# Kernel tuning notes

Measured on AMD Instinct MI355X. Metric: run time of the kernel, lower is better.

## Reference

```python
import jax, jax.numpy as jnp
import numpy as np

D_K = 64

def setup_inputs() -> dict:
    key = jax.random.key(0)
    k1, k2, k3 = jax.random.split(key, 3)
    B, H, S, d = 4, 16, 2048, D_K
    Q = jax.random.normal(k1, (B, H, S, d), dtype=jnp.float32)
    K = jax.random.normal(k2, (B, H, S, d), dtype=jnp.float32)
    V = jax.random.normal(k3, (B, H, S, d), dtype=jnp.float32)
    attn_mask = jnp.ones((1, 1, S, S), dtype=jnp.float32)
    return {"Q": Q, "K": K, "V": V, "attn_mask": attn_mask}

def reference(Q, K, V, attn_mask):
    # scores = Q K^T / sqrt(d_k)  -> [B, H, S, S]
    scale = 1.0 / np.sqrt(D_K).astype(np.float32)
    scores = jnp.einsum('bhqd,bhkd->bhqk', Q, K) * scale
    # unnormalized exp (NO max-subtraction, faithful to original)
    scores = jnp.exp(scores)
    # multiplicative mask applied POST-exp
    scores = scores * attn_mask
    # manual sum-normalization with eps
    attn = scores / (jnp.sum(scores, axis=-1, keepdims=True) + 1e-08)
    context = jnp.einsum('bhqk,bhkd->bhqd', attn, V)
    return (context, attn)
```

## Files before the change

kernel.cpp:

```cpp
#include <hip/hip_runtime.h>

#define S_LEN 2048
#define D_KD  64
#define NKT   32
#define NBH   64
#define KSEG  4

typedef __attribute__((ext_vector_type(8))) short short8;
typedef __attribute__((ext_vector_type(4))) float f32x4;

__device__ __forceinline__ unsigned short f2bf(float f) {
    unsigned u = __builtin_bit_cast(unsigned, f);
    return (unsigned short)((u + 0x7fffu + ((u >> 16) & 1u)) >> 16);
}

__device__ __forceinline__ void ldsbar() {
    asm volatile("s_waitcnt lgkmcnt(0)" ::: "memory");
    __builtin_amdgcn_s_barrier();
}
__device__ __forceinline__ void ldswait() {
    asm volatile("s_waitcnt lgkmcnt(0)" ::: "memory");
    __builtin_amdgcn_sched_barrier(0);
}

__device__ __forceinline__ unsigned swz(int row, int bytecol) {
    return (unsigned)(row * 128 + bytecol) ^
           (((((unsigned)row & 7u) ^ ((unsigned)row >> 3)) & 7u) << 4);
}

__device__ __forceinline__ void load_rm(const float* __restrict__ g,
                                        float4 r[4], int tid) {
#pragma unroll
    for (int j = 0; j < 4; j++) r[j] = *(const float4*)(g + j * 1024 + tid * 4);
}
__device__ __forceinline__ void write_rm(const float4 r[4],
                                         unsigned char* lds, int tid) {
#pragma unroll
    for (int j = 0; j < 4; j++) {
        int idx = j * 1024 + tid * 4;
        int row = idx >> 6, col = idx & 63;
        ushort4 b = make_ushort4(f2bf(r[j].x), f2bf(r[j].y), f2bf(r[j].z), f2bf(r[j].w));
        *(ushort4*)(lds + swz(row, col * 2)) = b;
    }
}
__device__ __forceinline__ void load_tr(const float* __restrict__ g,
                                        float4 r[4], int tid) {
    const int br = tid >> 4, bc = tid & 15;
    const float* gp = g + (4 * br) * 64 + 4 * bc;
#pragma unroll
    for (int j = 0; j < 4; j++) r[j] = *(const float4*)(gp + j * 64);
}
__device__ __forceinline__ void write_tr(const float4 r[4],
                                         unsigned char* lds, int tid) {
    const int br = tid >> 4, bc = tid & 15;
    ushort4 c;
    c = make_ushort4(f2bf(r[0].x), f2bf(r[1].x), f2bf(r[2].x), f2bf(r[3].x));
    *(ushort4*)(lds + swz(4 * bc + 0, 8 * br)) = c;
    c = make_ushort4(f2bf(r[0].y), f2bf(r[1].y), f2bf(r[2].y), f2bf(r[3].y));
    *(ushort4*)(lds + swz(4 * bc + 1, 8 * br)) = c;
    c = make_ushort4(f2bf(r[0].z), f2bf(r[1].z), f2bf(r[2].z), f2bf(r[3].z));
    *(ushort4*)(lds + swz(4 * bc + 2, 8 * br)) = c;
    c = make_ushort4(f2bf(r[0].w), f2bf(r[1].w), f2bf(r[2].w), f2bf(r[3].w));
    *(ushort4*)(lds + swz(4 * bc + 3, 8 * br)) = c;
}
__device__ __forceinline__ void stage_rm(const float* __restrict__ g,
                                         unsigned char* lds, int tid) {
    float4 r[4];
    load_rm(g, r, tid);
    write_rm(r, lds, tid);
}

__device__ __forceinline__ void qkt(const unsigned char* Qs, const unsigned char* Ks,
                                    int wv, int lr, int lg, f32x4 acc[4]) {
    short8 a0 = *(const short8*)(Qs + swz(16 * wv + lr, 16 * lg));
    short8 a1 = *(const short8*)(Qs + swz(16 * wv + lr, 16 * lg + 64));
#pragma unroll
    for (int nt = 0; nt < 4; nt++) {
        short8 b0 = *(const short8*)(Ks + swz(16 * nt + lr, 16 * lg));
        short8 b1 = *(const short8*)(Ks + swz(16 * nt + lr, 16 * lg + 64));
        acc[nt] = __builtin_amdgcn_mfma_f32_16x16x32_bf16(a0, b0, acc[nt], 0, 0, 0);
        acc[nt] = __builtin_amdgcn_mfma_f32_16x16x32_bf16(a1, b1, acc[nt], 0, 0, 0);
    }
}

__global__ __launch_bounds__(256) void attn_ctx(
    const float* __restrict__ Q, const float* __restrict__ K,
    const float* __restrict__ V, const float* __restrict__ M,
    float* __restrict__ out, float* __restrict__ invg) {
    __shared__ unsigned char Qs[8192];
    __shared__ unsigned char Ks[8192];
    __shared__ unsigned char Vs[8192];
    __shared__ unsigned char Ps[8192];

    const int tid = threadIdx.x;
    const int wv = tid >> 6, lane = tid & 63, lr = lane & 15, lg = lane >> 4;
    const int blk = blockIdx.x;
    const int bh = (blk & 7) * 8 + (blk >> 8);
    const int qt = (blk >> 3) & 31;

    const float* Qg = Q + ((size_t)bh * S_LEN + qt * 64) * D_KD;
    const float* Kg = K + (size_t)bh * S_LEN * D_KD;
    const float* Vg = V + (size_t)bh * S_LEN * D_KD;
    float* ctxg = out + ((size_t)bh * S_LEN + qt * 64) * D_KD;
    const float* Mg = M + (size_t)(qt * 64) * S_LEN;

    stage_rm(Qg, Qs, tid);

    f32x4 accc[4] = {};
    float rs[4] = {0.f, 0.f, 0.f, 0.f};

    float4 kreg[4], vreg[4];
    load_rm(Kg, kreg, tid);
    load_tr(Vg, vreg, tid);

    for (int t = 0; t < NKT; t++) {
        write_rm(kreg, Ks, tid);
        write_tr(vreg, Vs, tid);
        ldsbar();

        if (t + 1 < NKT) {
            load_rm(Kg + (size_t)(t + 1) * 64 * D_KD, kreg, tid);
            load_tr(Vg + (size_t)(t + 1) * 64 * D_KD, vreg, tid);
        }

        float mreg[4][4];
#pragma unroll
        for (int r = 0; r < 4; r++) {
            const float* mrow = Mg + (size_t)(16 * wv + 4 * lg + r) * S_LEN + t * 64;
#pragma unroll
            for (int nt = 0; nt < 4; nt++) mreg[r][nt] = mrow[16 * nt + lr];
        }

        f32x4 acc[4] = {};
        qkt(Qs, Ks, wv, lr, lg, acc);

#pragma unroll
        for (int r = 0; r < 4; r++) {
            const int row = 16 * wv + 4 * lg + r;
#pragma unroll
            for (int nt = 0; nt < 4; nt++) {
                float e = __expf(acc[nt][r] * 0.125f) * mreg[r][nt];
                rs[r] += e;
                *(unsigned short*)(Ps + swz(row, (16 * nt + lr) * 2)) = f2bf(e);
            }
        }
        ldswait();

#pragma unroll
        for (int kt = 0; kt < 2; kt++) {
            short8 pa = *(const short8*)(Ps + swz(16 * wv + lr, 16 * lg + 64 * kt));
#pragma unroll
            for (int nt = 0; nt < 4; nt++) {
                short8 vb = *(const short8*)(Vs + swz(16 * nt + lr, 16 * lg + 64 * kt));
                accc[nt] = __builtin_amdgcn_mfma_f32_16x16x32_bf16(pa, vb, accc[nt], 0, 0, 0);
            }
        }
        ldsbar();
    }

    float inv[4];
#pragma unroll
    for (int r = 0; r < 4; r++) {
        float v = rs[r];
        v += __shfl_xor(v, 1);
        v += __shfl_xor(v, 2);
        v += __shfl_xor(v, 4);
        v += __shfl_xor(v, 8);
        inv[r] = 1.0f / (v + 1e-8f);
    }

#pragma unroll
    for (int r = 0; r < 4; r++) {
        const int row = 16 * wv + 4 * lg + r;
#pragma unroll
        for (int nt = 0; nt < 4; nt++)
            ctxg[(size_t)row * D_KD + 16 * nt + lr] = accc[nt][r] * inv[r];
    }

    if (lr == 0) {
#pragma unroll
        for (int r = 0; r < 4; r++)
            invg[(size_t)bh * S_LEN + qt * 64 + 16 * wv + 4 * lg + r] = inv[r];
    }
}

__global__ __launch_bounds__(256) void attn_mat(
    const float* __restrict__ Q, const float* __restrict__ K,
    const float* __restrict__ M, const float* __restrict__ invg,
    float* __restrict__ out) {
    __shared__ unsigned char Qs[8192];
    __shared__ unsigned char Ks[8192];

    const int tid = threadIdx.x;
    const int wv = tid >> 6, lane = tid & 63, lr = lane & 15, lg = lane >> 4;
    const int ks = blockIdx.x & (KSEG - 1);
    const int qt = (blockIdx.x >> 2) & 31;
    const int bh = blockIdx.x >> 7;

    const float* Qg = Q + ((size_t)bh * S_LEN + qt * 64) * D_KD;
    const float* Kg = K + (size_t)bh * S_LEN * D_KD;
    const float* Mg = M + (size_t)(qt * 64) * S_LEN;
    float* attng = out + (size_t)NBH * S_LEN * D_KD +
                   (size_t)bh * S_LEN * S_LEN + (size_t)(qt * 64) * S_LEN;

    stage_rm(Qg, Qs, tid);

    float inv[4];
#pragma unroll
    for (int r = 0; r < 4; r++)
        inv[r] = invg[(size_t)bh * S_LEN + qt * 64 + 16 * wv + 4 * lg + r];

    const int nt_kt = S_LEN / (64 * KSEG);
    const float* Kseg = Kg + (size_t)(ks * (S_LEN / KSEG)) * D_KD;

    float4 kreg[4];
    load_rm(Kseg, kreg, tid);

    for (int kt = 0; kt < nt_kt; kt++) {
        const int key0 = ks * (S_LEN / KSEG) + kt * 64;
        write_rm(kreg, Ks, tid);
        ldsbar();

        if (kt + 1 < nt_kt)
            load_rm(Kseg + (size_t)(kt + 1) * 64 * D_KD, kreg, tid);

        float mreg[4][4];
#pragma unroll
        for (int r = 0; r < 4; r++) {
            const float* mrow = Mg + (size_t)(16 * wv + 4 * lg + r) * S_LEN + key0;
#pragma unroll
            for (int nt = 0; nt < 4; nt++) mreg[r][nt] = mrow[16 * nt + lr];
        }

        f32x4 acc[4] = {};
        qkt(Qs, Ks, wv, lr, lg, acc);

#pragma unroll
        for (int r = 0; r < 4; r++) {
            const int row = 16 * wv + 4 * lg + r;
            float* arow = attng + (size_t)row * S_LEN + key0;
#pragma unroll
            for (int nt = 0; nt < 4; nt++) {
                float e = __expf(acc[nt][r] * 0.125f) * mreg[r][nt] * inv[r];
                __builtin_nontemporal_store(e, arow + 16 * nt + lr);
            }
        }
        ldsbar();
    }
}

extern "C" void kernel_launch(void* const* d_in, const int* in_sizes, int n_in,
                              void* d_out, int out_size, void* d_ws, size_t ws_size,
                              hipStream_t stream) {
    const float* Q = (const float*)d_in[0];
    const float* K = (const float*)d_in[1];
    const float* V = (const float*)d_in[2];
    const float* M = (const float*)d_in[3];
    float* out = (float*)d_out;
    float* invg = (float*)d_ws;
    attn_ctx<<<dim3(NBH * 32), dim3(256), 0, stream>>>(Q, K, V, M, out, invg);
    attn_mat<<<dim3(NBH * 32 * KSEG), dim3(256), 0, stream>>>(Q, K, M, invg, out);
}
```

Baseline: 453.7 us.

## Pre-convert K/V to swizzled bf16 images in workspace before attention kernels

Adds a conversion kernel that converts K to bf16 and V to transposed bf16, writing both in the swizzled LDS tile layout into workspace. The attention kernels then copy those tiles straight into LDS with 16-byte loads instead of reloading fp32 and converting on every Q tile. The context kernel also keeps Q fragments in registers rather than staging them through LDS. This removes the repeated fp32 K/V reads and conversions, at the cost of one extra launch and a workspace round trip, and it falls back to the old path when workspace is too small.

```diff
diff --git a/kernel.cpp b/kernel.cpp
--- a/kernel.cpp
+++ b/kernel.cpp
@@ -13,6 +13,14 @@
     unsigned u = __builtin_bit_cast(unsigned, f);
     return (unsigned short)((u + 0x7fffu + ((u >> 16) & 1u)) >> 16);
 }
+__device__ __forceinline__ short8 pack8(float4 a, float4 b) {
+    short8 r;
+    r[0] = (short)f2bf(a.x); r[1] = (short)f2bf(a.y);
+    r[2] = (short)f2bf(a.z); r[3] = (short)f2bf(a.w);
+    r[4] = (short)f2bf(b.x); r[5] = (short)f2bf(b.y);
+    r[6] = (short)f2bf(b.z); r[7] = (short)f2bf(b.w);
+    return r;
+}
 
 __device__ __forceinline__ void ldsbar() {
     asm volatile("s_waitcnt lgkmcnt(0)" ::: "memory");
@@ -34,13 +42,13 @@
     for (int j = 0; j < 4; j++) r[j] = *(const float4*)(g + j * 1024 + tid * 4);
 }
 __device__ __forceinline__ void write_rm(const float4 r[4],
-                                         unsigned char* lds, int tid) {
+                                         unsigned char* dst, int tid) {
 #pragma unroll
     for (int j = 0; j < 4; j++) {
         int idx = j * 1024 + tid * 4;
         int row = idx >> 6, col = idx & 63;
         ushort4 b = make_ushort4(f2bf(r[j].x), f2bf(r[j].y), f2bf(r[j].z), f2bf(r[j].w));
-        *(ushort4*)(lds + swz(row, col * 2)) = b;
+        *(ushort4*)(dst + swz(row, col * 2)) = b;
     }
 }
 __device__ __forceinline__ void load_tr(const float* __restrict__ g,
@@ -51,17 +59,17 @@
     for (int j = 0; j < 4; j++) r[j] = *(const float4*)(gp + j * 64);
 }
 __device__ __forceinline__ void write_tr(const float4 r[4],
-                                         unsigned char* lds, int tid) {
+                                         unsigned char* dst, int tid) {
     const int br = tid >> 4, bc = tid & 15;
     ushort4 c;
     c = make_ushort4(f2bf(r[0].x), f2bf(r[1].x), f2bf(r[2].x), f2bf(r[3].x));
-    *(ushort4*)(lds + swz(4 * bc + 0, 8 * br)) = c;
+    *(ushort4*)(dst + swz(4 * bc + 0, 8 * br)) = c;
     c = make_ushort4(f2bf(r[0].y), f2bf(r[1].y), f2bf(r[2].y), f2bf(r[3].y));
-    *(ushort4*)(lds + swz(4 * bc + 1, 8 * br)) = c;
+    *(ushort4*)(dst + swz(4 * bc + 1, 8 * br)) = c;
     c = make_ushort4(f2bf(r[0].z), f2bf(r[1].z), f2bf(r[2].z), f2bf(r[3].z));
-    *(ushort4*)(lds + swz(4 * bc + 2, 8 * br)) = c;
+    *(ushort4*)(dst + swz(4 * bc + 2, 8 * br)) = c;
     c = make_ushort4(f2bf(r[0].w), f2bf(r[1].w), f2bf(r[2].w), f2bf(r[3].w));
-    *(ushort4*)(lds + swz(4 * bc + 3, 8 * br)) = c;
+    *(ushort4*)(dst + swz(4 * bc + 3, 8 * br)) = c;
 }
 __device__ __forceinline__ void stage_rm(const float* __restrict__ g,
                                          unsigned char* lds, int tid) {
@@ -82,8 +90,214 @@
         acc[nt] = __builtin_amdgcn_mfma_f32_16x16x32_bf16(a1, b1, acc[nt], 0, 0, 0);
     }
 }
-
-__global__ __launch_bounds__(256) void attn_ctx(
+__device__ __forceinline__ void qkt_r(short8 qa0, short8 qa1, const unsigned char* Ks,
+                                      int lr, int lg, f32x4 acc[4]) {
+#pragma unroll
+    for (int nt = 0; nt < 4; nt++) {
+        short8 b0 = *(const short8*)(Ks + swz(16 * nt + lr, 16 * lg));
+        short8 b1 = *(const short8*)(Ks + swz(16 * nt + lr, 16 * lg + 64));
+        acc[nt] = __builtin_amdgcn_mfma_f32_16x16x32_bf16(qa0, b0, acc[nt], 0, 0, 0);
+        acc[nt] = __builtin_amdgcn_mfma_f32_16x16x32_bf16(qa1, b1, acc[nt], 0, 0, 0);
+    }
+}
+
+__global__ __launch_bounds__(256) void conv_kv(
+    const float* __restrict__ K, const float* __restrict__ V,
+    unsigned char* __restrict__ wsK, unsigned char* __restrict__ wsV) {
+    const int blk = blockIdx.x;
+    const int bh = blk >> 5, t = blk & 31;
+    const int tid = threadIdx.x;
+    const float* Kg = K + ((size_t)bh * S_LEN + t * 64) * D_KD;
+    const float* Vg = V + ((size_t)bh * S_LEN + t * 64) * D_KD;
+    float4 r[4];
+    load_rm(Kg, r, tid);
+    write_rm(r, wsK + (size_t)blk * 8192, tid);
+    float4 v[4];
+    load_tr(Vg, v, tid);
+    write_tr(v, wsV + (size_t)blk * 8192, tid);
+}
+
+__global__ __launch_bounds__(256) void attn_ctx_pre(
+    const float* __restrict__ Q, const unsigned char* __restrict__ wsK,
+    const unsigned char* __restrict__ wsV, const float* __restrict__ M,
+    float* __restrict__ out, float* __restrict__ invg) {
+    __shared__ unsigned char Ks[8192];
+    __shared__ unsigned char Vs[8192];
+    __shared__ unsigned char Ps[8192];
+
+    const int tid = threadIdx.x;
+    const int wv = tid >> 6, lane = tid & 63, lr = lane & 15, lg = lane >> 4;
+    const int blk = blockIdx.x;
+    const int bh = (blk & 7) * 8 + (blk >> 8);
+    const int qt = (blk >> 3) & 31;
+
+    const unsigned char* Kimg = wsK + (size_t)(bh * 32) * 8192;
+    const unsigned char* Vimg = wsV + (size_t)(bh * 32) * 8192;
+    float* ctxg = out + ((size_t)bh * S_LEN + qt * 64) * D_KD;
+    const float* Mg = M + (size_t)(qt * 64) * S_LEN;
+
+    short8 qa0, qa1;
+    {
+        const float* qr = Q + ((size_t)bh * S_LEN + qt * 64 + 16 * wv + lr) * D_KD + 8 * lg;
+        qa0 = pack8(*(const float4*)(qr), *(const float4*)(qr + 4));
+        qa1 = pack8(*(const float4*)(qr + 32), *(const float4*)(qr + 36));
+    }
+
+    f32x4 accc[4] = {};
+    float rs[4] = {0.f, 0.f, 0.f, 0.f};
+
+    uint4 kr0, kr1, vr0, vr1;
+    kr0 = *(const uint4*)(Kimg + tid * 16);
+    kr1 = *(const uint4*)(Kimg + 4096 + tid * 16);
+    vr0 = *(const uint4*)(Vimg + tid * 16);
+    vr1 = *(const uint4*)(Vimg + 4096 + tid * 16);
+
+    for (int t = 0; t < NKT; t++) {
+        *(uint4*)(Ks + tid * 16) = kr0;
+        *(uint4*)(Ks + 4096 + tid * 16) = kr1;
+        *(uint4*)(Vs + tid * 16) = vr0;
+        *(uint4*)(Vs + 4096 + tid * 16) = vr1;
+        ldsbar();
+
+        if (t + 1 < NKT) {
+            const unsigned char* kn = Kimg + (size_t)(t + 1) * 8192;
+            const unsigned char* vn = Vimg + (size_t)(t + 1) * 8192;
+            kr0 = *(const uint4*)(kn + tid * 16);
+            kr1 = *(const uint4*)(kn + 4096 + tid * 16);
+            vr0 = *(const uint4*)(vn + tid * 16);
+            vr1 = *(const uint4*)(vn + 4096 + tid * 16);
+        }
+
+        float mreg[4][4];
+#pragma unroll
+        for (int r = 0; r < 4; r++) {
+            const float* mrow = Mg + (size_t)(16 * wv + 4 * lg + r) * S_LEN + t * 64;
+#pragma unroll
+            for (int nt = 0; nt < 4; nt++) mreg[r][nt] = mrow[16 * nt + lr];
+        }
+
+        f32x4 acc[4] = {};
+        qkt_r(qa0, qa1, Ks, lr, lg, acc);
+
+#pragma unroll
+        for (int r = 0; r < 4; r++) {
+            const int row = 16 * wv + 4 * lg + r;
+#pragma unroll
+            for (int nt = 0; nt < 4; nt++) {
+                float e = __expf(acc[nt][r] * 0.125f) * mreg[r][nt];
+                rs[r] += e;
+                *(unsigned short*)(Ps + swz(row, (16 * nt + lr) * 2)) = f2bf(e);
+            }
+        }
+        ldswait();
+
+#pragma unroll
+        for (int kt = 0; kt < 2; kt++) {
+            short8 pa = *(const short8*)(Ps + swz(16 * wv + lr, 16 * lg + 64 * kt));
+#pragma unroll
+            for (int nt = 0; nt < 4; nt++) {
+                short8 vb = *(const short8*)(Vs + swz(16 * nt + lr, 16 * lg + 64 * kt));
+                accc[nt] = __builtin_amdgcn_mfma_f32_16x16x32_bf16(pa, vb, accc[nt], 0, 0, 0);
+            }
+        }
+        ldsbar();
+    }
+
+    float inv[4];
+#pragma unroll
+    for (int r = 0; r < 4; r++) {
+        float v = rs[r];
+        v += __shfl_xor(v, 1);
+        v += __shfl_xor(v, 2);
+        v += __shfl_xor(v, 4);
+        v += __shfl_xor(v, 8);
+        inv[r] = 1.0f / (v + 1e-8f);
+    }
+
+#pragma unroll
+    for (int r = 0; r < 4; r++) {
+        const int row = 16 * wv + 4 * lg + r;
+#pragma unroll
+        for (int nt = 0; nt < 4; nt++)
+            ctxg[(size_t)row * D_KD + 16 * nt + lr] = accc[nt][r] * inv[r];
+    }
+
+    if (lr == 0) {
+#pragma unroll
+        for (int r = 0; r < 4; r++)
+            invg[(size_t)bh * S_LEN + qt * 64 + 16 * wv + 4 * lg + r] = inv[r];
+    }
+}
+
+__global__ __launch_bounds__(256) void attn_mat_pre(
+    const float* __restrict__ Q, const unsigned char* __restrict__ wsK,
+    const float* __restrict__ M, const float* __restrict__ invg,
+    float* __restrict__ out) {
+    __shared__ unsigned char Qs[8192];
+    __shared__ unsigned char Ks[8192];
+
+    const int tid = threadIdx.x;
+    const int wv = tid >> 6, lane = tid & 63, lr = lane & 15, lg = lane >> 4;
+    const int ks = blockIdx.x & (KSEG - 1);
+    const int qt = (blockIdx.x >> 2) & 31;
+    const int bh = blockIdx.x >> 7;
+
+    const float* Qg = Q + ((size_t)bh * S_LEN + qt * 64) * D_KD;
+    const unsigned char* Kimg = wsK + (size_t)(bh * 32 + ks * 8) * 8192;
+    const float* Mg = M + (size_t)(qt * 64) * S_LEN;
+    float* attng = out + (size_t)NBH * S_LEN * D_KD +
+                   (size_t)bh * S_LEN * S_LEN + (size_t)(qt * 64) * S_LEN;
+
+    stage_rm(Qg, Qs, tid);
+
+    float inv[4];
+#pragma unroll
+    for (int r = 0; r < 4; r++)
+        inv[r] = invg[(size_t)bh * S_LEN + qt * 64 + 16 * wv + 4 * lg + r];
+
+    const int nt_kt = S_LEN / (64 * KSEG);
+
+    uint4 kr0 = *(const uint4*)(Kimg + tid * 16);
+    uint4 kr1 = *(const uint4*)(Kimg + 4096 + tid * 16);
+
+    for (int kt = 0; kt < nt_kt; kt++) {
+        const int key0 = ks * (S_LEN / KSEG) + kt * 64;
+        *(uint4*)(Ks + tid * 16) = kr0;
+        *(uint4*)(Ks + 4096 + tid * 16) = kr1;
+        ldsbar();
+
+        if (kt + 1 < nt_kt) {
+            const unsigned char* kn = Kimg + (size_t)(kt + 1) * 8192;
+            kr0 = *(const uint4*)(kn + tid * 16);
+            kr1 = *(const uint4*)(kn + 4096 + tid * 16);
+        }
+
+        float mreg[4][4];
+#pragma unroll
+        for (int r = 0; r < 4; r++) {
+            const float* mrow = Mg + (size_t)(16 * wv + 4 * lg + r) * S_LEN + key0;
+#pragma unroll
+            for (int nt = 0; nt < 4; nt++) mreg[r][nt] = mrow[16 * nt + lr];
+        }
+
+        f32x4 acc[4] = {};
+        qkt(Qs, Ks, wv, lr, lg, acc);
+
+#pragma unroll
+        for (int r = 0; r < 4; r++) {
+            const int row = 16 * wv + 4 * lg + r;
+            float* arow = attng + (size_t)row * S_LEN + key0;
+#pragma unroll
+            for (int nt = 0; nt < 4; nt++) {
+                float e = __expf(acc[nt][r] * 0.125f) * mreg[r][nt] * inv[r];
+                __builtin_nontemporal_store(e, arow + 16 * nt + lr);
+            }
+        }
+        ldsbar();
+    }
+}
+
+__global__ __launch_bounds__(256) void attn_ctx_v11(
     const float* __restrict__ Q, const float* __restrict__ K,
     const float* __restrict__ V, const float* __restrict__ M,
     float* __restrict__ out, float* __restrict__ invg) {
@@ -105,10 +319,8 @@
     const float* Mg = M + (size_t)(qt * 64) * S_LEN;
 
     stage_rm(Qg, Qs, tid);
-
     f32x4 accc[4] = {};
     float rs[4] = {0.f, 0.f, 0.f, 0.f};
-
     float4 kreg[4], vreg[4];
     load_rm(Kg, kreg, tid);
     load_tr(Vg, vreg, tid);
@@ -117,12 +329,10 @@
         write_rm(kreg, Ks, tid);
         write_tr(vreg, Vs, tid);
         ldsbar();
-
         if (t + 1 < NKT) {
             load_rm(Kg + (size_t)(t + 1) * 64 * D_KD, kreg, tid);
             load_tr(Vg + (size_t)(t + 1) * 64 * D_KD, vreg, tid);
         }
-
         float mreg[4][4];
 #pragma unroll
         for (int r = 0; r < 4; r++) {
@@ -130,10 +340,8 @@
 #pragma unroll
             for (int nt = 0; nt < 4; nt++) mreg[r][nt] = mrow[16 * nt + lr];
         }
-
         f32x4 acc[4] = {};
         qkt(Qs, Ks, wv, lr, lg, acc);
-
 #pragma unroll
         for (int r = 0; r < 4; r++) {
             const int row = 16 * wv + 4 * lg + r;
@@ -145,7 +353,6 @@
             }
         }
         ldswait();
-
 #pragma unroll
         for (int kt = 0; kt < 2; kt++) {
             short8 pa = *(const short8*)(Ps + swz(16 * wv + lr, 16 * lg + 64 * kt));
@@ -157,7 +364,6 @@
         }
         ldsbar();
     }
-
     float inv[4];
 #pragma unroll
     for (int r = 0; r < 4; r++) {
@@ -168,7 +374,6 @@
         v += __shfl_xor(v, 8);
         inv[r] = 1.0f / (v + 1e-8f);
     }
-
 #pragma unroll
     for (int r = 0; r < 4; r++) {
         const int row = 16 * wv + 4 * lg + r;
@@ -176,7 +381,6 @@
         for (int nt = 0; nt < 4; nt++)
             ctxg[(size_t)row * D_KD + 16 * nt + lr] = accc[nt][r] * inv[r];
     }
-
     if (lr == 0) {
 #pragma unroll
         for (int r = 0; r < 4; r++)
@@ -184,7 +388,7 @@
     }
 }
 
-__global__ __launch_bounds__(256) void attn_mat(
+__global__ __launch_bounds__(256) void attn_mat_v11(
     const float* __restrict__ Q, const float* __restrict__ K,
     const float* __restrict__ M, const float* __restrict__ invg,
     float* __restrict__ out) {
@@ -204,7 +408,6 @@
                    (size_t)bh * S_LEN * S_LEN + (size_t)(qt * 64) * S_LEN;
 
     stage_rm(Qg, Qs, tid);
-
     float inv[4];
 #pragma unroll
     for (int r = 0; r < 4; r++)
@@ -212,7 +415,6 @@
 
     const int nt_kt = S_LEN / (64 * KSEG);
     const float* Kseg = Kg + (size_t)(ks * (S_LEN / KSEG)) * D_KD;
-
     float4 kreg[4];
     load_rm(Kseg, kreg, tid);
 
@@ -220,10 +422,8 @@
         const int key0 = ks * (S_LEN / KSEG) + kt * 64;
         write_rm(kreg, Ks, tid);
         ldsbar();
-
         if (kt + 1 < nt_kt)
             load_rm(Kseg + (size_t)(kt + 1) * 64 * D_KD, kreg, tid);
-
         float mreg[4][4];
 #pragma unroll
         for (int r = 0; r < 4; r++) {
@@ -231,10 +431,8 @@
 #pragma unroll
             for (int nt = 0; nt < 4; nt++) mreg[r][nt] = mrow[16 * nt + lr];
         }
-
         f32x4 acc[4] = {};
         qkt(Qs, Ks, wv, lr, lg, acc);
-
 #pragma unroll
         for (int r = 0; r < 4; r++) {
             const int row = 16 * wv + 4 * lg + r;
@@ -257,7 +455,18 @@
     const float* V = (const float*)d_in[2];
     const float* M = (const float*)d_in[3];
     float* out = (float*)d_out;
-    float* invg = (float*)d_ws;
-    attn_ctx<<<dim3(NBH * 32), dim3(256), 0, stream>>>(Q, K, V, M, out, invg);
-    attn_mat<<<dim3(NBH * 32 * KSEG), dim3(256), 0, stream>>>(Q, K, M, invg, out);
-}
+    unsigned char* wsb = (unsigned char*)d_ws;
+    float* invg = (float*)wsb;
+    unsigned char* wsK = wsb + 512 * 1024;
+    unsigned char* wsV = wsK + (size_t)NBH * 32 * 8192;
+    const size_t need = 512 * 1024 + 2 * (size_t)NBH * 32 * 8192;
+
+    if (ws_size >= need) {
+        conv_kv<<<dim3(NBH * 32), dim3(256), 0, stream>>>(K, V, wsK, wsV);
+        attn_ctx_pre<<<dim3(NBH * 32), dim3(256), 0, stream>>>(Q, wsK, wsV, M, out, invg);
+        attn_mat_pre<<<dim3(NBH * 32 * KSEG), dim3(256), 0, stream>>>(Q, wsK, M, invg, out);
+    } else {
+        attn_ctx_v11<<<dim3(NBH * 32), dim3(256), 0, stream>>>(Q, K, V, M, out, invg);
+        attn_mat_v11<<<dim3(NBH * 32 * KSEG), dim3(256), 0, stream>>>(Q, K, M, invg, out);
+    }
+}
```

Result: slower. 547.2 us (+20.6%).

## Keep P in registers via transposed MFMA and permlane swaps, drop Q/P LDS

Applied to the files above, without the earlier changes.

The context kernel now computes S^T = K·Q^T, so each lane holds a column of scores. It repacks the exp'd probabilities into the B-operand layout of the PV MFMA with permlane32/16 swaps rather than a round-trip through a shared-memory P buffer. Q is held in registers as bf16 fragments, which removes the Q and P LDS arrays and the mid-tile LDS wait. It also vectorises the mask loads and context stores to float4 and adds an occupancy hint to launch_bounds. This trades extra cross-lane permute and select instructions and register pressure for less LDS traffic and higher occupancy.

```diff
diff --git a/kernel.cpp b/kernel.cpp
--- a/kernel.cpp
+++ b/kernel.cpp
@@ -8,19 +8,55 @@
 
 typedef __attribute__((ext_vector_type(8))) short short8;
 typedef __attribute__((ext_vector_type(4))) float f32x4;
+typedef __attribute__((ext_vector_type(4))) unsigned u32x4;
+typedef __attribute__((ext_vector_type(2))) int int2v;
 
 __device__ __forceinline__ unsigned short f2bf(float f) {
     unsigned u = __builtin_bit_cast(unsigned, f);
     return (unsigned short)((u + 0x7fffu + ((u >> 16) & 1u)) >> 16);
 }
+__device__ __forceinline__ unsigned pack2(float a, float b) {
+    return (unsigned)f2bf(a) | ((unsigned)f2bf(b) << 16);
+}
+__device__ __forceinline__ short8 pack8(float4 a, float4 b) {
+    short8 r;
+    r[0] = (short)f2bf(a.x); r[1] = (short)f2bf(a.y);
+    r[2] = (short)f2bf(a.z); r[3] = (short)f2bf(a.w);
+    r[4] = (short)f2bf(b.x); r[5] = (short)f2bf(b.y);
+    r[6] = (short)f2bf(b.z); r[7] = (short)f2bf(b.w);
+    return r;
+}
 
 __device__ __forceinline__ void ldsbar() {
     asm volatile("s_waitcnt lgkmcnt(0)" ::: "memory");
     __builtin_amdgcn_s_barrier();
 }
-__device__ __forceinline__ void ldswait() {
-    asm volatile("s_waitcnt lgkmcnt(0)" ::: "memory");
-    __builtin_amdgcn_sched_barrier(0);
+
+__device__ __forceinline__ void swap32(unsigned e0, unsigned e1,
+                                       unsigned& a, unsigned& b, int lane) {
+#if __has_builtin(__builtin_amdgcn_permlane32_swap)
+    int2v r = __builtin_amdgcn_permlane32_swap((int)e0, (int)e1, false, false);
+    a = (unsigned)r[0];
+    b = (unsigned)r[1];
+#else
+    unsigned t0 = __shfl_xor(e0, 32), t1 = __shfl_xor(e1, 32);
+    const bool hi = lane >= 32;
+    a = hi ? t1 : e0;
+    b = hi ? e1 : t0;
+#endif
+}
+__device__ __forceinline__ void swap16(unsigned x, unsigned& p, unsigned& q,
+                                       int lane) {
+#if __has_builtin(__builtin_amdgcn_permlane16_swap)
+    int2v r = __builtin_amdgcn_permlane16_swap((int)x, (int)x, false, false);
+    p = (unsigned)r[0];
+    q = (unsigned)r[1];
+#else
+    unsigned t = __shfl_xor(x, 16);
+    const bool odd = (lane >> 4) & 1;
+    p = odd ? t : x;
+    q = odd ? x : t;
+#endif
 }
 
 __device__ __forceinline__ unsigned swz(int row, int bytecol) {
@@ -83,14 +119,12 @@
     }
 }
 
-__global__ __launch_bounds__(256) void attn_ctx(
+__global__ __launch_bounds__(256, 4) void attn_ctx(
     const float* __restrict__ Q, const float* __restrict__ K,
     const float* __restrict__ V, const float* __restrict__ M,
     float* __restrict__ out, float* __restrict__ invg) {
-    __shared__ unsigned char Qs[8192];
     __shared__ unsigned char Ks[8192];
     __shared__ unsigned char Vs[8192];
-    __shared__ unsigned char Ps[8192];
 
     const int tid = threadIdx.x;
     const int wv = tid >> 6, lane = tid & 63, lr = lane & 15, lg = lane >> 4;
@@ -98,16 +132,20 @@
     const int bh = (blk & 7) * 8 + (blk >> 8);
     const int qt = (blk >> 3) & 31;
 
-    const float* Qg = Q + ((size_t)bh * S_LEN + qt * 64) * D_KD;
     const float* Kg = K + (size_t)bh * S_LEN * D_KD;
     const float* Vg = V + (size_t)bh * S_LEN * D_KD;
     float* ctxg = out + ((size_t)bh * S_LEN + qt * 64) * D_KD;
     const float* Mg = M + (size_t)(qt * 64) * S_LEN;
 
-    stage_rm(Qg, Qs, tid);
-
-    f32x4 accc[4] = {};
-    float rs[4] = {0.f, 0.f, 0.f, 0.f};
+    short8 qa0, qa1;
+    {
+        const float* qr = Q + ((size_t)bh * S_LEN + qt * 64 + 16 * wv + lr) * D_KD + 8 * lg;
+        qa0 = pack8(*(const float4*)(qr), *(const float4*)(qr + 4));
+        qa1 = pack8(*(const float4*)(qr + 32), *(const float4*)(qr + 36));
+    }
+
+    f32x4 acc_ctx[4] = {};
+    float rs = 0.f;
 
     float4 kreg[4], vreg[4];
     load_rm(Kg, kreg, tid);
@@ -123,65 +161,76 @@
             load_tr(Vg + (size_t)(t + 1) * 64 * D_KD, vreg, tid);
         }
 
-        float mreg[4][4];
-#pragma unroll
-        for (int r = 0; r < 4; r++) {
-            const float* mrow = Mg + (size_t)(16 * wv + 4 * lg + r) * S_LEN + t * 64;
-#pragma unroll
-            for (int nt = 0; nt < 4; nt++) mreg[r][nt] = mrow[16 * nt + lr];
-        }
-
-        f32x4 acc[4] = {};
-        qkt(Qs, Ks, wv, lr, lg, acc);
-
-#pragma unroll
-        for (int r = 0; r < 4; r++) {
-            const int row = 16 * wv + 4 * lg + r;
-#pragma unroll
-            for (int nt = 0; nt < 4; nt++) {
-                float e = __expf(acc[nt][r] * 0.125f) * mreg[r][nt];
-                rs[r] += e;
-                *(unsigned short*)(Ps + swz(row, (16 * nt + lr) * 2)) = f2bf(e);
+        float4 m4[4];
+        const float* mbase = Mg + (size_t)(16 * wv + lr) * S_LEN + t * 64 + 4 * lg;
+#pragma unroll
+        for (int nt = 0; nt < 4; nt++) m4[nt] = *(const float4*)(mbase + 16 * nt);
+
+        f32x4 sc[4] = {};
+#pragma unroll
+        for (int nt = 0; nt < 4; nt++) {
+            short8 kb0 = *(const short8*)(Ks + swz(16 * nt + lr, 16 * lg));
+            short8 kb1 = *(const short8*)(Ks + swz(16 * nt + lr, 16 * lg + 64));
+            sc[nt] = __builtin_amdgcn_mfma_f32_16x16x32_bf16(kb0, qa0, sc[nt], 0, 0, 0);
+            sc[nt] = __builtin_amdgcn_mfma_f32_16x16x32_bf16(kb1, qa1, sc[nt], 0, 0, 0);
+        }
+
+        float e[4][4];
+        unsigned E[4][2];
+#pragma unroll
+        for (int nt = 0; nt < 4; nt++) {
+#pragma unroll
+            for (int r = 0; r < 4; r++) {
+                float v = __expf(sc[nt][r] * 0.125f) *
+                          ((const float*)&m4[nt])[r];
+                e[nt][r] = v;
+                rs += v;
             }
-        }
-        ldswait();
-
-#pragma unroll
-        for (int kt = 0; kt < 2; kt++) {
-            short8 pa = *(const short8*)(Ps + swz(16 * wv + lr, 16 * lg + 64 * kt));
-#pragma unroll
-            for (int nt = 0; nt < 4; nt++) {
-                short8 vb = *(const short8*)(Vs + swz(16 * nt + lr, 16 * lg + 64 * kt));
-                accc[nt] = __builtin_amdgcn_mfma_f32_16x16x32_bf16(pa, vb, accc[nt], 0, 0, 0);
+            E[nt][0] = pack2(e[nt][0], e[nt][1]);
+            E[nt][1] = pack2(e[nt][2], e[nt][3]);
+        }
+
+        short8 pb[2];
+#pragma unroll
+        for (int kh = 0; kh < 2; kh++) {
+            unsigned w[4];
+#pragma unroll
+            for (int c = 0; c < 2; c++) {
+                unsigned nA, nB, pA, qA, pB, qB;
+                swap32(E[2 * kh][c], E[2 * kh + 1][c], nA, nB, lane);
+                swap16(nA, pA, qA, lane);
+                swap16(nB, pB, qB, lane);
+                const bool lodd = (lg & 1);
+                w[c] = lodd ? pB : pA;
+                w[2 + c] = lodd ? qB : qA;
             }
+            u32x4 t4 = {w[0], w[1], w[2], w[3]};
+            pb[kh] = __builtin_bit_cast(short8, t4);
+        }
+
+#pragma unroll
+        for (int dt = 0; dt < 4; dt++) {
+            short8 v0 = *(const short8*)(Vs + swz(16 * dt + lr, 16 * lg));
+            short8 v1 = *(const short8*)(Vs + swz(16 * dt + lr, 16 * lg + 64));
+            acc_ctx[dt] = __builtin_amdgcn_mfma_f32_16x16x32_bf16(v0, pb[0], acc_ctx[dt], 0, 0, 0);
+            acc_ctx[dt] = __builtin_amdgcn_mfma_f32_16x16x32_bf16(v1, pb[1], acc_ctx[dt], 0, 0, 0);
         }
         ldsbar();
     }
 
-    float inv[4];
-#pragma unroll
-    for (int r = 0; r < 4; r++) {
-        float v = rs[r];
-        v += __shfl_xor(v, 1);
-        v += __shfl_xor(v, 2);
-        v += __shfl_xor(v, 4);
-        v += __shfl_xor(v, 8);
-        inv[r] = 1.0f / (v + 1e-8f);
-    }
-
-#pragma unroll
-    for (int r = 0; r < 4; r++) {
-        const int row = 16 * wv + 4 * lg + r;
-#pragma unroll
-        for (int nt = 0; nt < 4; nt++)
-            ctxg[(size_t)row * D_KD + 16 * nt + lr] = accc[nt][r] * inv[r];
-    }
-
-    if (lr == 0) {
-#pragma unroll
-        for (int r = 0; r < 4; r++)
-            invg[(size_t)bh * S_LEN + qt * 64 + 16 * wv + 4 * lg + r] = inv[r];
-    }
+    float v = rs;
+    v += __shfl_xor(v, 16);
+    v += __shfl_xor(v, 32);
+    const float inv = 1.0f / (v + 1e-8f);
+
+#pragma unroll
+    for (int dt = 0; dt < 4; dt++) {
+        float4 o = make_float4(acc_ctx[dt][0] * inv, acc_ctx[dt][1] * inv,
+                               acc_ctx[dt][2] * inv, acc_ctx[dt][3] * inv);
+        *(float4*)(ctxg + (size_t)(16 * wv + lr) * D_KD + 16 * dt + 4 * lg) = o;
+    }
+    if (lg == 0)
+        invg[(size_t)bh * S_LEN + qt * 64 + 16 * wv + lr] = inv;
 }
 
 __global__ __launch_bounds__(256) void attn_mat(
```

Measured after the change: 493.6 us. +8.8%, slower.

## Pre-scan mask tiles and skip mask loads for all-ones tiles

Applied to the files above, without the earlier changes.

Adds a mask_scan kernel that records, for each 64x64 tile of the mask, whether every element equals 1.0. Both the context and attention-matrix kernels read these flags through a ballot and skip the per-element mask loads and multiplies on all-ones tiles. Tiles that are not all ones still take the original masked path. This removes repeated reads of the 16 MB mask across all batch-heads, at the cost of an extra kernel launch, a full mask read each call, and some branch code.

```diff
diff --git a/kernel.cpp b/kernel.cpp
--- a/kernel.cpp
+++ b/kernel.cpp
@@ -83,10 +83,30 @@
     }
 }
 
+__global__ __launch_bounds__(256) void mask_scan(
+    const float* __restrict__ M, unsigned char* __restrict__ flags) {
+    __shared__ int ok4[4];
+    const int tid = threadIdx.x;
+    const int rt = blockIdx.x >> 5, ct = blockIdx.x & 31;
+    const float* p = M + (size_t)(rt * 64 + (tid >> 2)) * S_LEN + ct * 64 + (tid & 3) * 16;
+    bool ones = true;
+#pragma unroll
+    for (int j = 0; j < 4; j++) {
+        float4 v = *(const float4*)(p + 4 * j);
+        ones = ones && (v.x == 1.0f) && (v.y == 1.0f) && (v.z == 1.0f) && (v.w == 1.0f);
+    }
+    bool wall = __all(ones);
+    if ((tid & 63) == 0) ok4[tid >> 6] = wall ? 1 : 0;
+    __syncthreads();
+    if (tid == 0)
+        flags[blockIdx.x] = (unsigned char)(ok4[0] & ok4[1] & ok4[2] & ok4[3]);
+}
+
 __global__ __launch_bounds__(256) void attn_ctx(
     const float* __restrict__ Q, const float* __restrict__ K,
     const float* __restrict__ V, const float* __restrict__ M,
-    float* __restrict__ out, float* __restrict__ invg) {
+    float* __restrict__ out, float* __restrict__ invg,
+    const unsigned char* __restrict__ mflags) {
     __shared__ unsigned char Qs[8192];
     __shared__ unsigned char Ks[8192];
     __shared__ unsigned char Vs[8192];
@@ -104,6 +124,9 @@
     float* ctxg = out + ((size_t)bh * S_LEN + qt * 64) * D_KD;
     const float* Mg = M + (size_t)(qt * 64) * S_LEN;
 
+    unsigned long long bl = __ballot(lane < 32 && mflags[qt * 32 + (lane & 31)] != 0);
+    const unsigned mmask = (unsigned)bl;
+
     stage_rm(Qg, Qs, tid);
 
     f32x4 accc[4] = {};
@@ -123,25 +146,39 @@
             load_tr(Vg + (size_t)(t + 1) * 64 * D_KD, vreg, tid);
         }
 
-        float mreg[4][4];
-#pragma unroll
-        for (int r = 0; r < 4; r++) {
-            const float* mrow = Mg + (size_t)(16 * wv + 4 * lg + r) * S_LEN + t * 64;
-#pragma unroll
-            for (int nt = 0; nt < 4; nt++) mreg[r][nt] = mrow[16 * nt + lr];
-        }
+        const bool mones = (mmask >> t) & 1u;
 
         f32x4 acc[4] = {};
         qkt(Qs, Ks, wv, lr, lg, acc);
 
-#pragma unroll
-        for (int r = 0; r < 4; r++) {
-            const int row = 16 * wv + 4 * lg + r;
-#pragma unroll
-            for (int nt = 0; nt < 4; nt++) {
-                float e = __expf(acc[nt][r] * 0.125f) * mreg[r][nt];
-                rs[r] += e;
-                *(unsigned short*)(Ps + swz(row, (16 * nt + lr) * 2)) = f2bf(e);
+        if (mones) {
+#pragma unroll
+            for (int r = 0; r < 4; r++) {
+                const int row = 16 * wv + 4 * lg + r;
+#pragma unroll
+                for (int nt = 0; nt < 4; nt++) {
+                    float e = __expf(acc[nt][r] * 0.125f);
+                    rs[r] += e;
+                    *(unsigned short*)(Ps + swz(row, (16 * nt + lr) * 2)) = f2bf(e);
+                }
+            }
+        } else {
+            float mreg[4][4];
+#pragma unroll
+            for (int r = 0; r < 4; r++) {
+                const float* mrow = Mg + (size_t)(16 * wv + 4 * lg + r) * S_LEN + t * 64;
+#pragma unroll
+                for (int nt = 0; nt < 4; nt++) mreg[r][nt] = mrow[16 * nt + lr];
+            }
+#pragma unroll
+            for (int r = 0; r < 4; r++) {
+                const int row = 16 * wv + 4 * lg + r;
+#pragma unroll
+                for (int nt = 0; nt < 4; nt++) {
+                    float e = __expf(acc[nt][r] * 0.125f) * mreg[r][nt];
+                    rs[r] += e;
+                    *(unsigned short*)(Ps + swz(row, (16 * nt + lr) * 2)) = f2bf(e);
+                }
             }
         }
         ldswait();
@@ -187,7 +224,7 @@
 __global__ __launch_bounds__(256) void attn_mat(
     const float* __restrict__ Q, const float* __restrict__ K,
     const float* __restrict__ M, const float* __restrict__ invg,
-    float* __restrict__ out) {
+    float* __restrict__ out, const unsigned char* __restrict__ mflags) {
     __shared__ unsigned char Qs[8192];
     __shared__ unsigned char Ks[8192];
 
@@ -203,6 +240,9 @@
     float* attng = out + (size_t)NBH * S_LEN * D_KD +
                    (size_t)bh * S_LEN * S_LEN + (size_t)(qt * 64) * S_LEN;
 
+    unsigned long long bl = __ballot(lane < 32 && mflags[qt * 32 + (lane & 31)] != 0);
+    const unsigned mmask = (unsigned)bl;
+
     stage_rm(Qg, Qs, tid);
 
     float inv[4];
@@ -224,25 +264,39 @@
         if (kt + 1 < nt_kt)
             load_rm(Kseg + (size_t)(kt + 1) * 64 * D_KD, kreg, tid);
 
-        float mreg[4][4];
-#pragma unroll
-        for (int r = 0; r < 4; r++) {
-            const float* mrow = Mg + (size_t)(16 * wv + 4 * lg + r) * S_LEN + key0;
-#pragma unroll
-            for (int nt = 0; nt < 4; nt++) mreg[r][nt] = mrow[16 * nt + lr];
-        }
+        const bool mones = (mmask >> (ks * 8 + kt)) & 1u;
 
         f32x4 acc[4] = {};
         qkt(Qs, Ks, wv, lr, lg, acc);
 
-#pragma unroll
-        for (int r = 0; r < 4; r++) {
-            const int row = 16 * wv + 4 * lg + r;
-            float* arow = attng + (size_t)row * S_LEN + key0;
-#pragma unroll
-            for (int nt = 0; nt < 4; nt++) {
-                float e = __expf(acc[nt][r] * 0.125f) * mreg[r][nt] * inv[r];
-                __builtin_nontemporal_store(e, arow + 16 * nt + lr);
+        if (mones) {
+#pragma unroll
+            for (int r = 0; r < 4; r++) {
+                const int row = 16 * wv + 4 * lg + r;
+                float* arow = attng + (size_t)row * S_LEN + key0;
+#pragma unroll
+                for (int nt = 0; nt < 4; nt++) {
+                    float e = __expf(acc[nt][r] * 0.125f) * inv[r];
+                    __builtin_nontemporal_store(e, arow + 16 * nt + lr);
+                }
+            }
+        } else {
+            float mreg[4][4];
+#pragma unroll
+            for (int r = 0; r < 4; r++) {
+                const float* mrow = Mg + (size_t)(16 * wv + 4 * lg + r) * S_LEN + key0;
+#pragma unroll
+                for (int nt = 0; nt < 4; nt++) mreg[r][nt] = mrow[16 * nt + lr];
+            }
+#pragma unroll
+            for (int r = 0; r < 4; r++) {
+                const int row = 16 * wv + 4 * lg + r;
+                float* arow = attng + (size_t)row * S_LEN + key0;
+#pragma unroll
+                for (int nt = 0; nt < 4; nt++) {
+                    float e = __expf(acc[nt][r] * 0.125f) * mreg[r][nt] * inv[r];
+                    __builtin_nontemporal_store(e, arow + 16 * nt + lr);
+                }
             }
         }
         ldsbar();
@@ -257,7 +311,11 @@
     const float* V = (const float*)d_in[2];
     const float* M = (const float*)d_in[3];
     float* out = (float*)d_out;
-    float* invg = (float*)d_ws;
-    attn_ctx<<<dim3(NBH * 32), dim3(256), 0, stream>>>(Q, K, V, M, out, invg);
-    attn_mat<<<dim3(NBH * 32 * KSEG), dim3(256), 0, stream>>>(Q, K, M, invg, out);
-}
+    unsigned char* wsb = (unsigned char*)d_ws;
+    float* invg = (float*)wsb;
+    unsigned char* mflags = wsb + 512 * 1024;
+
+    mask_scan<<<dim3(1024), dim3(256), 0, stream>>>(M, mflags);
+    attn_ctx<<<dim3(NBH * 32), dim3(256), 0, stream>>>(Q, K, V, M, out, invg, mflags);
+    attn_mat<<<dim3(NBH * 32 * KSEG), dim3(256), 0, stream>>>(Q, K, M, invg, out, mflags);
+}
```

Result: slower. 555.3 us (+22.4%).
